# Optimization experiments

Measured on AMD Instinct MI355X. Metric: run time of the kernel, lower is better.

## Reference

```python
import jax, jax.numpy as jnp
import numpy as np

B, S_IMG, S_TXT, D, H = 1, 2304, 512, 3072, 24
HD = D // H  # 128


def setup_inputs() -> dict:
    key = jax.random.key(0)
    ks = jax.random.split(key, 24)
    inp = {
        'hidden_states': jax.random.normal(ks[0], (B, S_IMG, D), jnp.float32),
        'encoder_hidden_states': jax.random.normal(ks[1], (B, S_TXT, D), jnp.float32),
    }
    wnames = ['wq', 'wk', 'wv', 'waq', 'wak', 'wav']
    for i, n in enumerate(wnames):
        inp[n] = jax.random.normal(ks[2 + i], (D, D), jnp.float32) * 0.02
        inp['b' + n[1:]] = jnp.zeros((D,), jnp.float32)
    for n in ['nq', 'nk', 'naq', 'nak']:
        inp[n] = jnp.ones((HD,), jnp.float32)
    inp['w_out'] = jax.random.normal(ks[8], (D, D), jnp.float32) * 0.02
    inp['b_out'] = jnp.zeros((D,), jnp.float32)
    inp['w_add_out'] = jax.random.normal(ks[9], (D, D), jnp.float32) * 0.02
    inp['b_add_out'] = jnp.zeros((D,), jnp.float32)
    # RoPE: complex freqs_cis of shape [seq, HD//2]; store cos/sin parts
    two_pi = 2.0 * np.pi
    ang_img = jax.random.uniform(ks[10], (S_IMG, HD // 2), jnp.float32) * two_pi
    ang_txt = jax.random.uniform(ks[11], (S_TXT, HD // 2), jnp.float32) * two_pi
    inp['img_cos'], inp['img_sin'] = jnp.cos(ang_img), jnp.sin(ang_img)
    inp['txt_cos'], inp['txt_sin'] = jnp.cos(ang_txt), jnp.sin(ang_txt)
    return inp


def _rms(x, w, eps=1e-6):
    return x * jax.lax.rsqrt(jnp.mean(x * x, axis=-1, keepdims=True) + eps) * w


def _rope(x, cos, sin):
    # x: [B,S,H,HD]; complex multiply on consecutive pairs (use_real=False path)
    xr = x.reshape(*x.shape[:-1], HD // 2, 2)
    a, b = xr[..., 0], xr[..., 1]
    c = cos[None, :, None, :]
    s = sin[None, :, None, :]
    out = jnp.stack([a * c - b * s, a * s + b * c], axis=-1)
    return out.reshape(x.shape)


def reference(hidden_states, encoder_hidden_states,
              wq, bq, wk, bk, wv, bv, waq, baq, wak, bak, wav, bav,
              nq, nk, naq, nak, w_out, b_out, w_add_out, b_add_out,
              img_cos, img_sin, txt_cos, txt_sin):
    def proj(x, w, b):
        return x @ w.T + b

    def heads(x):
        return x.reshape(x.shape[0], x.shape[1], H, HD)

    img_q = _rope(_rms(heads(proj(hidden_states, wq, bq)), nq), img_cos, img_sin)
    img_k = _rope(_rms(heads(proj(hidden_states, wk, bk)), nk), img_cos, img_sin)
    img_v = heads(proj(hidden_states, wv, bv))
    txt_q = _rope(_rms(heads(proj(encoder_hidden_states, waq, baq)), naq), txt_cos, txt_sin)
    txt_k = _rope(_rms(heads(proj(encoder_hidden_states, wak, bak)), nak), txt_cos, txt_sin)
    txt_v = heads(proj(encoder_hidden_states, wav, bav))

    q = jnp.concatenate([txt_q, img_q], axis=1)  # [B, S_TXT+S_IMG, H, HD]
    k = jnp.concatenate([txt_k, img_k], axis=1)
    v = jnp.concatenate([txt_v, img_v], axis=1)

    scale = 1.0 / jnp.sqrt(jnp.float32(HD))
    scores = jnp.einsum('bqhd,bkhd->bhqk', q, k) * scale
    attn = jax.nn.softmax(scores, axis=-1)
    out = jnp.einsum('bhqk,bkhd->bqhd', attn, v)
    out = out.reshape(out.shape[0], out.shape[1], D)

    txt_o = out[:, :S_TXT, :]
    img_o = out[:, S_TXT:, :]
    img_attn_output = img_o @ w_out.T + b_out
    txt_attn_output = txt_o @ w_add_out.T + b_add_out
    return (img_attn_output, txt_attn_output)
```

## Files before the change

### kernel.cpp

```cpp
#include <hip/hip_runtime.h>

#define S_IMG 2304
#define S_TXT 512
#define S_ALL 2816
#define DMODEL 3072
#define NH 24
#define HD 128
#define N3 9216

typedef _Float16 half8 __attribute__((ext_vector_type(8)));
typedef _Float16 half4 __attribute__((ext_vector_type(4)));
typedef _Float16 half2v __attribute__((ext_vector_type(2)));
typedef float float4v __attribute__((ext_vector_type(4)));

__device__ __forceinline__ void gld_lds16(const _Float16* g, _Float16* l) {
  __builtin_amdgcn_global_load_lds(
      (const __attribute__((address_space(1))) unsigned int*)g,
      (__attribute__((address_space(3))) unsigned int*)l, 16, 0, 0);
}

__device__ __forceinline__ float4v mfma16(half8 a, half8 b, float4v c) {
  return __builtin_amdgcn_mfma_f32_16x16x32_f16(a, b, c, 0, 0, 0);
}

__global__ __launch_bounds__(256) void cast_f32_f16(const float* __restrict__ src,
                                                    _Float16* __restrict__ dst, int n8) {
  int i = blockIdx.x * 256 + threadIdx.x;
  if (i >= n8) return;
  float4v a = ((const float4v*)src)[2 * i];
  float4v b = ((const float4v*)src)[2 * i + 1];
  half8 h;
  h[0] = (_Float16)a[0]; h[1] = (_Float16)a[1]; h[2] = (_Float16)a[2]; h[3] = (_Float16)a[3];
  h[4] = (_Float16)b[0]; h[5] = (_Float16)b[1]; h[6] = (_Float16)b[2]; h[7] = (_Float16)b[3];
  ((half8*)dst)[i] = h;
}

__global__ __launch_bounds__(256) void bias_pack(const float* __restrict__ bq, const float* __restrict__ bk,
                                                 const float* __restrict__ bv, const float* __restrict__ baq,
                                                 const float* __restrict__ bak, const float* __restrict__ bav,
                                                 float* __restrict__ b3i, float* __restrict__ b3t) {
  int i = blockIdx.x * 256 + threadIdx.x;
  int j = i % 9216;
  const float* src;
  if (i < 9216) src = (j < 3072) ? bq : (j < 6144) ? bk : bv;
  else          src = (j < 3072) ? baq : (j < 6144) ? bak : bav;
  float v = src[j & 3071];
  if (i < 9216) b3i[j] = v; else b3t[j] = v;
}

template <typename OT>
__global__ __launch_bounds__(256) void gemm_f16(const _Float16* __restrict__ A,
                                                const _Float16* __restrict__ W,
                                                const float* __restrict__ bias,
                                                OT* __restrict__ C,
                                                int M, int N, int K) {
  __shared__ __align__(16) _Float16 As[128 * 32];
  __shared__ __align__(16) _Float16 Ws[128 * 32];
  const int tid = threadIdx.x;
  const int wave = tid >> 6, lane = tid & 63;
  const int quad = lane >> 4, col = lane & 15;
  const int wm = (wave >> 1) * 64, wn = (wave & 1) * 64;
  const size_t bm = (size_t)blockIdx.y * 128, bn = (size_t)blockIdx.x * 128;
  const _Float16* Ag = A + (bm + (tid >> 2)) * (size_t)K + (tid & 3) * 8;
  const _Float16* Wg = W + (bn + (tid >> 2)) * (size_t)K + (tid & 3) * 8;

  float4v acc[4][4];
#pragma unroll
  for (int mt = 0; mt < 4; mt++)
#pragma unroll
    for (int nt = 0; nt < 4; nt++) acc[mt][nt] = (float4v){0.f, 0.f, 0.f, 0.f};

  for (int k0 = 0; k0 < K; k0 += 32) {
    gld_lds16(Ag + k0, As + tid * 8);
    gld_lds16(Ag + (size_t)64 * K + k0, As + 2048 + tid * 8);
    gld_lds16(Wg + k0, Ws + tid * 8);
    gld_lds16(Wg + (size_t)64 * K + k0, Ws + 2048 + tid * 8);
    __syncthreads();
    half8 af[4], bf[4];
#pragma unroll
    for (int mt = 0; mt < 4; mt++)
      af[mt] = *(const half8*)&As[(wm + mt * 16 + col) * 32 + quad * 8];
#pragma unroll
    for (int nt = 0; nt < 4; nt++)
      bf[nt] = *(const half8*)&Ws[(wn + nt * 16 + col) * 32 + quad * 8];
#pragma unroll
    for (int mt = 0; mt < 4; mt++)
#pragma unroll
      for (int nt = 0; nt < 4; nt++)
        acc[mt][nt] = mfma16(af[mt], bf[nt], acc[mt][nt]);
    __syncthreads();
  }
#pragma unroll
  for (int mt = 0; mt < 4; mt++)
#pragma unroll
    for (int nt = 0; nt < 4; nt++) {
      const size_t gn = bn + wn + nt * 16 + col;
      const float b = bias[gn];
      const size_t gr = bm + wm + mt * 16 + quad * 4;
#pragma unroll
      for (int i = 0; i < 4; i++)
        C[(gr + i) * (size_t)N + gn] = (OT)(acc[mt][nt][i] + b);
    }
}

__global__ __launch_bounds__(256) void rmsrope(const _Float16* __restrict__ QKV,
                                               const float* __restrict__ nq, const float* __restrict__ nk,
                                               const float* __restrict__ naq, const float* __restrict__ nak,
                                               const float* __restrict__ icos, const float* __restrict__ isin,
                                               const float* __restrict__ tcos, const float* __restrict__ tsin,
                                               _Float16* __restrict__ Qh,
                                               _Float16* __restrict__ Kh) {
  const float SC = 0.08838834764831845f * 1.4426950408889634f;
  const int wg = blockIdx.x * 4 + (threadIdx.x >> 6);
  const int lane = threadIdx.x & 63;
  const int h = wg % NH;
  const int s = wg / NH;
  const bool is_txt = s < S_TXT;
  const float* nwq = is_txt ? naq : nq;
  const float* nwk = is_txt ? nak : nk;
  const int sr = is_txt ? s : s - S_TXT;
  const float* ct = is_txt ? tcos : icos;
  const float* st = is_txt ? tsin : isin;
  const float cs = ct[sr * 64 + lane];
  const float sn = st[sr * 64 + lane];
  const size_t base = (size_t)s * N3 + h * HD + 2 * lane;
  const half2v q2 = *(const half2v*)&QKV[base];
  const half2v k2 = *(const half2v*)&QKV[base + DMODEL];
  const float qx = (float)q2[0], qy = (float)q2[1];
  const float kx = (float)k2[0], ky = (float)k2[1];
  float sq = qx * qx + qy * qy;
  float sk = kx * kx + ky * ky;
#pragma unroll
  for (int m2 = 32; m2 >= 1; m2 >>= 1) {
    sq += __shfl_xor(sq, m2);
    sk += __shfl_xor(sk, m2);
  }
  const float rq = rsqrtf(sq * (1.f / 128.f) + 1e-6f) * SC;
  const float rk = rsqrtf(sk * (1.f / 128.f) + 1e-6f);
  float wa = nwq[2 * lane], wb = nwq[2 * lane + 1];
  float a = qx * rq * wa, b = qy * rq * wb;
  half2v qo = {(_Float16)(a * cs - b * sn), (_Float16)(a * sn + b * cs)};
  wa = nwk[2 * lane]; wb = nwk[2 * lane + 1];
  a = kx * rk * wa; b = ky * rk * wb;
  half2v ko = {(_Float16)(a * cs - b * sn), (_Float16)(a * sn + b * cs)};
  const size_t ob = ((size_t)h * S_ALL + s) * HD + 2 * lane;
  *(half2v*)&Qh[ob] = qo;
  *(half2v*)&Kh[ob] = ko;
}

__global__ __launch_bounds__(256) void v_transpose(const _Float16* __restrict__ Vraw,
                                                   _Float16* __restrict__ Vt) {
  __shared__ _Float16 T[64][72];
  const int t = threadIdx.x;
  const int sb = blockIdx.x, db = blockIdx.y, h = blockIdx.z;
  const _Float16* src = Vraw + (size_t)(sb * 64) * N3 + h * HD + db * 64;
#pragma unroll
  for (int it = 0; it < 4; it++) {
    int r = it * 16 + (t >> 4);
    int c = (t & 15) * 4;
    *(half4*)&T[r][c] = *(const half4*)(src + (size_t)r * N3 + c);
  }
  __syncthreads();
  _Float16* dst = Vt + ((size_t)h * HD + db * 64) * S_ALL + sb * 64;
#pragma unroll
  for (int it = 0; it < 4; it++) {
    int r = it * 16 + (t >> 4);
    int c = (t & 15) * 4;
    half4 o;
    o[0] = T[c][r]; o[1] = T[c + 1][r];
    o[2] = T[c + 2][r]; o[3] = T[c + 3][r];
    *(half4*)(dst + (size_t)r * S_ALL + c) = o;
  }
}

__global__ __launch_bounds__(256, 3) void attn_kernel(const _Float16* __restrict__ Qh,
                                                      const _Float16* __restrict__ Kh,
                                                      const _Float16* __restrict__ Vt,
                                                      _Float16* __restrict__ O) {
  __shared__ __align__(16) _Float16 Ks[4 * 64 * 32];
  __shared__ __align__(16) _Float16 Vs[2 * 128 * 32];
  __shared__ __align__(16) _Float16 Ps[4 * 2 * 2 * 512];
  const int tid = threadIdx.x;
  const int wave = tid >> 6, lane = tid & 63;
  const int quad = lane >> 4, col = lane & 15;
  const int h = blockIdx.y;
  const int q0 = blockIdx.x * 128;
  const _Float16* Qg = Qh + ((size_t)h * S_ALL + q0) * HD;
  const _Float16* Kg = Kh + (size_t)h * S_ALL * HD;
  const _Float16* Vg = Vt + (size_t)h * HD * S_ALL;

  const int fr = (col >> 1) & 3;
  const int srow = tid >> 2;
  const int schunk = (tid & 3) ^ ((tid >> 3) & 3);

  half8 qf[2][4];
#pragma unroll
  for (int mt = 0; mt < 2; mt++)
#pragma unroll
    for (int ks = 0; ks < 4; ks++)
      qf[mt][ks] = *(const half8*)(Qg + (size_t)(wave * 32 + mt * 16 + col) * HD + ks * 32 + quad * 8);

  float l_i[2][4];
  float4v oacc[2][8];
#pragma unroll
  for (int mt = 0; mt < 2; mt++) {
#pragma unroll
    for (int i = 0; i < 4; i++) l_i[mt][i] = 0.f;
#pragma unroll
    for (int nt = 0; nt < 8; nt++) oacc[mt][nt] = (float4v){0.f, 0.f, 0.f, 0.f};
  }

  _Float16* Pw = &Ps[wave * 2048];

  for (int kt = 0; kt < S_ALL / 64; kt++) {
    if (kt > 0) __syncthreads();
    const int base = kt * 64;
#pragma unroll
    for (int j = 0; j < 4; j++) {
      gld_lds16(Kg + (size_t)(base + srow) * HD + j * 32 + schunk * 8,
                Ks + j * 2048 + tid * 8);
      const int vrow = ((j & 1) * 256 + tid) >> 2;
      gld_lds16(Vg + (size_t)vrow * S_ALL + base + (j >> 1) * 32 + schunk * 8,
                Vs + j * 2048 + tid * 8);
    }
    __syncthreads();

#pragma unroll
    for (int nt = 0; nt < 4; nt++) {
      float4v sf0 = (float4v){0.f, 0.f, 0.f, 0.f};
      float4v sf1 = (float4v){0.f, 0.f, 0.f, 0.f};
#pragma unroll
      for (int ks = 0; ks < 4; ks++) {
        half8 kf = *(const half8*)&Ks[ks * 2048 + (nt * 16 + col) * 32 + (quad ^ fr) * 8];
        sf0 = mfma16(qf[0][ks], kf, sf0);
        sf1 = mfma16(qf[1][ks], kf, sf1);
      }
#pragma unroll
      for (int mt = 0; mt < 2; mt++) {
        _Float16* Pt = Pw + mt * 1024 + (nt >> 1) * 512;
#pragma unroll
        for (int i = 0; i < 4; i++) {
          const float s = (mt == 0) ? sf0[i] : sf1[i];
          const float p = exp2f(s - 2.0f);
          l_i[mt][i] += p;
          const int q = quad * 4 + i;
          const int slot = ((nt & 1) * 2 + (col >> 3)) ^ ((q >> 1) & 3);
          Pt[q * 32 + slot * 8 + (col & 7)] = (_Float16)p;
        }
      }
    }
    asm volatile("s_waitcnt lgkmcnt(0)" ::: "memory");
    __builtin_amdgcn_sched_barrier(0);
#pragma unroll
    for (int ks = 0; ks < 2; ks++) {
      half8 pf0 = *(const half8*)&Pw[ks * 512 + col * 32 + (quad ^ fr) * 8];
      half8 pf1 = *(const half8*)&Pw[1024 + ks * 512 + col * 32 + (quad ^ fr) * 8];
#pragma unroll
      for (int nt = 0; nt < 8; nt++) {
        half8 vf = *(const half8*)&Vs[ks * 4096 + (nt * 16 + col) * 32 + (quad ^ fr) * 8];
        oacc[0][nt] = mfma16(pf0, vf, oacc[0][nt]);
        oacc[1][nt] = mfma16(pf1, vf, oacc[1][nt]);
      }
    }
  }
#pragma unroll
  for (int mt = 0; mt < 2; mt++)
#pragma unroll
    for (int i = 0; i < 4; i++) {
      float l = l_i[mt][i];
      l += __shfl_xor(l, 1);
      l += __shfl_xor(l, 2);
      l += __shfl_xor(l, 4);
      l += __shfl_xor(l, 8);
      l_i[mt][i] = 1.0f / l;
    }
#pragma unroll
  for (int mt = 0; mt < 2; mt++)
#pragma unroll
    for (int nt = 0; nt < 8; nt++)
#pragma unroll
      for (int i = 0; i < 4; i++) {
        const int s = q0 + wave * 32 + mt * 16 + quad * 4 + i;
        O[(size_t)s * DMODEL + h * HD + nt * 16 + col] = (_Float16)(oacc[mt][nt][i] * l_i[mt][i]);
      }
}

extern "C" void kernel_launch(void* const* d_in, const int* in_sizes, int n_in,
                              void* d_out, int out_size, void* d_ws, size_t ws_size,
                              hipStream_t stream) {
  const float* hs   = (const float*)d_in[0];
  const float* ehs  = (const float*)d_in[1];
  const float* wq   = (const float*)d_in[2];
  const float* bq   = (const float*)d_in[3];
  const float* wk   = (const float*)d_in[4];
  const float* bk   = (const float*)d_in[5];
  const float* wv   = (const float*)d_in[6];
  const float* bv   = (const float*)d_in[7];
  const float* waq  = (const float*)d_in[8];
  const float* baq  = (const float*)d_in[9];
  const float* wak  = (const float*)d_in[10];
  const float* bak  = (const float*)d_in[11];
  const float* wav  = (const float*)d_in[12];
  const float* bav  = (const float*)d_in[13];
  const float* nq   = (const float*)d_in[14];
  const float* nk   = (const float*)d_in[15];
  const float* naq  = (const float*)d_in[16];
  const float* nak  = (const float*)d_in[17];
  const float* wo   = (const float*)d_in[18];
  const float* bo   = (const float*)d_in[19];
  const float* wao  = (const float*)d_in[20];
  const float* bao  = (const float*)d_in[21];
  const float* icos = (const float*)d_in[22];
  const float* isin = (const float*)d_in[23];
  const float* tcos = (const float*)d_in[24];
  const float* tsin = (const float*)d_in[25];

  char* w = (char*)d_ws;
  _Float16* wbuf = (_Float16*)(w + 0);
  _Float16* qh   = wbuf;
  _Float16* kh   = (_Float16*)(w + 17301504);
  _Float16* xi   = (_Float16*)(w + 56623104);
  _Float16* xt   = (_Float16*)(w + 70778880);
  _Float16* ob   = (_Float16*)(w + 56623104);
  float*    b3i  = (float*)(w + 73924608);
  float*    b3t  = (float*)(w + 73961472);
  _Float16* qkv  = (_Float16*)(w + 73998336);
  _Float16* vt   = (_Float16*)(w + 125902848);
  float* out = (float*)d_out;

  const size_t WSZ = (size_t)DMODEL * DMODEL;

  cast_f32_f16<<<3456, 256, 0, stream>>>(hs, xi, 884736);
  cast_f32_f16<<<768, 256, 0, stream>>>(ehs, xt, 196608);
  bias_pack<<<72, 256, 0, stream>>>(bq, bk, bv, baq, bak, bav, b3i, b3t);

  cast_f32_f16<<<4608, 256, 0, stream>>>(wq, wbuf, WSZ / 8);
  cast_f32_f16<<<4608, 256, 0, stream>>>(wk, wbuf + WSZ, WSZ / 8);
  cast_f32_f16<<<4608, 256, 0, stream>>>(wv, wbuf + 2 * WSZ, WSZ / 8);
  gemm_f16<_Float16><<<dim3(72, 18), 256, 0, stream>>>(xi, wbuf, b3i, qkv + (size_t)512 * N3, 2304, N3, DMODEL);
  cast_f32_f16<<<4608, 256, 0, stream>>>(waq, wbuf, WSZ / 8);
  cast_f32_f16<<<4608, 256, 0, stream>>>(wak, wbuf + WSZ, WSZ / 8);
  cast_f32_f16<<<4608, 256, 0, stream>>>(wav, wbuf + 2 * WSZ, WSZ / 8);
  gemm_f16<_Float16><<<dim3(72, 4), 256, 0, stream>>>(xt, wbuf, b3t, qkv, 512, N3, DMODEL);

  rmsrope<<<16896, 256, 0, stream>>>(qkv, nq, nk, naq, nak, icos, isin, tcos, tsin, qh, kh);
  v_transpose<<<dim3(44, 2, 24), 256, 0, stream>>>(qkv + 2 * DMODEL, vt);
  attn_kernel<<<dim3(22, 24), 256, 0, stream>>>(qh, kh, vt, ob);

  _Float16* wo16 = (_Float16*)(w + 73998336);
  cast_f32_f16<<<4608, 256, 0, stream>>>(wo, wo16, WSZ / 8);
  gemm_f16<float><<<dim3(24, 18), 256, 0, stream>>>(ob + (size_t)512 * DMODEL, wo16, bo, out, 2304, DMODEL, DMODEL);
  cast_f32_f16<<<4608, 256, 0, stream>>>(wao, wo16, WSZ / 8);
  gemm_f16<float><<<dim3(24, 4), 256, 0, stream>>>(ob, wo16, bao, out + (size_t)2304 * DMODEL, 512, DMODEL, DMODEL);
}
```

Baseline: 963.0 us.

## Add 256x256-tile double-buffered GEMM and merge output projections into one launch

Introduces a new 512-thread GEMM core with 256x256 output tiles, XOR-swizzled LDS staged by direct global-to-LDS loads, and a double-buffered K loop. It applies this core to the image QKV projection and to both output projections, which are now issued as a single launch. Blocks are remapped so that neighbouring tiles land on the same XCD, which is meant to improve L2 reuse. The larger tiles raise arithmetic intensity and cut launch count, but they use 128KB of LDS per block and many accumulators, so occupancy drops. Only 324 and 132 blocks launch, which may leave CUs underused in the wave tail.

```diff
diff --git a/kernel.cpp b/kernel.cpp
--- a/kernel.cpp
+++ b/kernel.cpp
@@ -21,6 +21,12 @@
 
 __device__ __forceinline__ float4v mfma16(half8 a, half8 b, float4v c) {
   return __builtin_amdgcn_mfma_f32_16x16x32_f16(a, b, c, 0, 0, 0);
+}
+
+__device__ __forceinline__ int xcd_swz(int bid, int nwg) {
+  const int q = nwg >> 3, r = nwg & 7;
+  const int x = bid & 7, l = bid >> 3;
+  return (x < r ? x * (q + 1) : r * (q + 1) + (x - r) * q) + l;
 }
 
 __global__ __launch_bounds__(256) void cast_f32_f16(const float* __restrict__ src,
@@ -101,6 +107,136 @@
       for (int i = 0; i < 4; i++)
         C[(gr + i) * (size_t)N + gn] = (OT)(acc[mt][nt][i] + b);
     }
+}
+
+template <typename OT>
+__device__ __forceinline__ void gemm256_core(const _Float16* __restrict__ A0,
+                                             const _Float16* __restrict__ W0,
+                                             const float* __restrict__ bias0,
+                                             OT* __restrict__ C0,
+                                             int K, int ldc) {
+  __shared__ __align__(16) _Float16 Asm[2][16384];
+  __shared__ __align__(16) _Float16 Wsm[2][16384];
+  const int tid = threadIdx.x;
+  const int wave = tid >> 6, lane = tid & 63;
+  const int quad = lane >> 4, col = lane & 15;
+  const int wm = (wave >> 2) * 128;
+  const int wn = (wave & 3) * 64;
+  const int srow = tid >> 3;
+  const int dst = tid * 8;
+  const _Float16* Asrc = A0 + (size_t)srow * K + (((tid & 7) ^ (srow & 7)) * 8);
+  const _Float16* Wsrc = W0 + (size_t)srow * K + (((tid & 7) ^ (srow & 7)) * 8);
+
+  auto stage = [&](int b, int k0) {
+#pragma unroll
+    for (int r = 0; r < 4; r++) {
+      gld_lds16(Asrc + (size_t)(r * 64) * K + k0, &Asm[b][r * 4096 + dst]);
+      gld_lds16(Wsrc + (size_t)(r * 64) * K + k0, &Wsm[b][r * 4096 + dst]);
+    }
+  };
+
+  float4v acc[8][4];
+#pragma unroll
+  for (int mr = 0; mr < 8; mr++)
+#pragma unroll
+    for (int nr = 0; nr < 4; nr++) acc[mr][nr] = (float4v){0.f, 0.f, 0.f, 0.f};
+
+  const int NT = K >> 6;
+  stage(0, 0);
+
+  for (int kt = 0; kt < NT; kt++) {
+    const int c = kt & 1;
+    asm volatile("" ::: "memory");
+    __builtin_amdgcn_s_barrier();
+    asm volatile("" ::: "memory");
+    if (kt + 1 < NT) {
+      stage(c ^ 1, (kt + 1) << 6);
+      asm volatile("s_waitcnt vmcnt(8)" ::: "memory");
+    } else {
+      asm volatile("s_waitcnt vmcnt(0)" ::: "memory");
+    }
+    asm volatile("" ::: "memory");
+    __builtin_amdgcn_s_barrier();
+    asm volatile("" ::: "memory");
+    const _Float16* Ab = Asm[c];
+    const _Float16* Wb = Wsm[c];
+#pragma unroll
+    for (int ph = 0; ph < 4; ph++) {
+      const int mh = ph >> 1, nh = ph & 1;
+      half8 af[4][2], bf[2][2];
+#pragma unroll
+      for (int i = 0; i < 4; i++)
+#pragma unroll
+        for (int kk = 0; kk < 2; kk++)
+          af[i][kk] = *(const half8*)&Ab[(wm + mh * 64 + i * 16 + col) * 64 +
+                                         (((kk << 2) | quad) ^ (col & 7)) * 8];
+#pragma unroll
+      for (int j = 0; j < 2; j++)
+#pragma unroll
+        for (int kk = 0; kk < 2; kk++)
+          bf[j][kk] = *(const half8*)&Wb[(wn + nh * 32 + j * 16 + col) * 64 +
+                                         (((kk << 2) | quad) ^ (col & 7)) * 8];
+      __builtin_amdgcn_s_setprio(1);
+#pragma unroll
+      for (int kk = 0; kk < 2; kk++)
+#pragma unroll
+        for (int i = 0; i < 4; i++)
+#pragma unroll
+          for (int j = 0; j < 2; j++)
+            acc[mh * 4 + i][nh * 2 + j] = mfma16(af[i][kk], bf[j][kk], acc[mh * 4 + i][nh * 2 + j]);
+      __builtin_amdgcn_s_setprio(0);
+    }
+  }
+#pragma unroll
+  for (int nr = 0; nr < 4; nr++) {
+    const int gn = wn + nr * 16 + col;
+    const float bv = bias0[gn];
+#pragma unroll
+    for (int mr = 0; mr < 8; mr++) {
+      const int gr = wm + mr * 16 + quad * 4;
+#pragma unroll
+      for (int ii = 0; ii < 4; ii++)
+        C0[(size_t)(gr + ii) * ldc + gn] = (OT)(acc[mr][nr][ii] + bv);
+    }
+  }
+}
+
+__global__ __launch_bounds__(512, 2) void gemm256_qkv(const _Float16* __restrict__ A,
+                                                      const _Float16* __restrict__ W,
+                                                      const float* __restrict__ bias,
+                                                      _Float16* __restrict__ C) {
+  const int wgid = xcd_swz(blockIdx.x, 36 * 9);
+  const int bx = wgid / 9, by = wgid % 9;
+  gemm256_core<_Float16>(A + (size_t)by * 256 * 3072,
+                         W + (size_t)bx * 256 * 3072,
+                         bias + bx * 256,
+                         C + (size_t)by * 256 * 9216 + bx * 256,
+                         3072, 9216);
+}
+
+__global__ __launch_bounds__(512, 2) void gemm256_out(const _Float16* __restrict__ ob,
+                                                      const _Float16* __restrict__ wo16,
+                                                      const float* __restrict__ bo,
+                                                      const _Float16* __restrict__ wao16,
+                                                      const float* __restrict__ bao,
+                                                      float* __restrict__ out) {
+  const int wgid = xcd_swz(blockIdx.x, 12 * 11);
+  const int bx = wgid / 11, by = wgid % 11;
+  const _Float16* A;
+  const _Float16* W;
+  const float* bias;
+  float* C;
+  if (by < 9) {
+    A = ob + ((size_t)512 + (size_t)by * 256) * 3072;
+    W = wo16; bias = bo;
+    C = out + (size_t)by * 256 * 3072;
+  } else {
+    A = ob + (size_t)(by - 9) * 256 * 3072;
+    W = wao16; bias = bao;
+    C = out + (size_t)2304 * 3072 + (size_t)(by - 9) * 256 * 3072;
+  }
+  gemm256_core<float>(A, W + (size_t)bx * 256 * 3072, bias + bx * 256, C + bx * 256,
+                      3072, 3072);
 }
 
 __global__ __launch_bounds__(256) void rmsrope(const _Float16* __restrict__ QKV,
@@ -337,7 +473,7 @@
   cast_f32_f16<<<4608, 256, 0, stream>>>(wq, wbuf, WSZ / 8);
   cast_f32_f16<<<4608, 256, 0, stream>>>(wk, wbuf + WSZ, WSZ / 8);
   cast_f32_f16<<<4608, 256, 0, stream>>>(wv, wbuf + 2 * WSZ, WSZ / 8);
-  gemm_f16<_Float16><<<dim3(72, 18), 256, 0, stream>>>(xi, wbuf, b3i, qkv + (size_t)512 * N3, 2304, N3, DMODEL);
+  gemm256_qkv<<<324, 512, 0, stream>>>(xi, wbuf, b3i, qkv + (size_t)512 * N3);
   cast_f32_f16<<<4608, 256, 0, stream>>>(waq, wbuf, WSZ / 8);
   cast_f32_f16<<<4608, 256, 0, stream>>>(wak, wbuf + WSZ, WSZ / 8);
   cast_f32_f16<<<4608, 256, 0, stream>>>(wav, wbuf + 2 * WSZ, WSZ / 8);
@@ -347,9 +483,9 @@
   v_transpose<<<dim3(44, 2, 24), 256, 0, stream>>>(qkv + 2 * DMODEL, vt);
   attn_kernel<<<dim3(22, 24), 256, 0, stream>>>(qh, kh, vt, ob);
 
-  _Float16* wo16 = (_Float16*)(w + 73998336);
+  _Float16* wo16  = (_Float16*)(w + 73998336);
+  _Float16* wao16 = wo16 + WSZ;
   cast_f32_f16<<<4608, 256, 0, stream>>>(wo, wo16, WSZ / 8);
-  gemm_f16<float><<<dim3(24, 18), 256, 0, stream>>>(ob + (size_t)512 * DMODEL, wo16, bo, out, 2304, DMODEL, DMODEL);
-  cast_f32_f16<<<4608, 256, 0, stream>>>(wao, wo16, WSZ / 8);
-  gemm_f16<float><<<dim3(24, 4), 256, 0, stream>>>(ob, wo16, bao, out + (size_t)2304 * DMODEL, 512, DMODEL, DMODEL);
-}
+  cast_f32_f16<<<4608, 256, 0, stream>>>(wao, wao16, WSZ / 8);
+  gemm256_out<<<132, 512, 0, stream>>>(ob, wo16, bo, wao16, bao, out);
+}
```

New measurement: 946.5 us. No clear change (-1.7%).
